# Kernel tuning notes

Hardware: AMD Instinct MI355X
Metric: run time of the kernel (lower is better)

## Reference

```python
import jax, jax.numpy as jnp
import numpy as np

H_IMG = 256; W_IMG = 256; C = 256
WIN = (16, 16); STRIPE = (32, 32); DF = 4; NH = 4
ASZ = (STRIPE[0] // DF, STRIPE[1] // DF)
TS = ((STRIPE[0] + ASZ[0]) // 2, (STRIPE[1] + ASZ[1]) // 2)  # stripe bias table half-size (20,20)


def _win_part(x, ws):
    # (B,H,W,c) -> (B*nW, ws0*ws1, c)
    B, H, W, c = x.shape
    x = x.reshape(B, H // ws[0], ws[0], W // ws[1], ws[1], c)
    return x.transpose(0, 1, 3, 2, 4, 5).reshape(-1, ws[0] * ws[1], c)


def _win_rev(w, ws, H, W):
    c = w.shape[-1]
    B = w.shape[0] // ((H // ws[0]) * (W // ws[1]))
    x = w.reshape(B, H // ws[0], W // ws[1], ws[0], ws[1], c)
    return x.transpose(0, 1, 3, 2, 4, 5).reshape(B, H, W, c)


def _l2n(x):
    # F.normalize(dim=-1)
    return x / jnp.maximum(jnp.linalg.norm(x, axis=-1, keepdims=True), 1e-12)


def _affine(attn, logit_scale, w1, b1, w2, table, index):
    # attn: (B_, nH, N1, N2); AffineTransform with mask=None
    N1, N2 = attn.shape[-2], attn.shape[-1]
    attn = attn * jnp.exp(jnp.minimum(logit_scale, np.log(100.0)))  # clamp max=log(1/0.01)
    bt = jax.nn.relu(table.reshape(-1, 2) @ w1 + b1) @ w2  # (T, nH)
    bias = bt[index.reshape(-1)].reshape(N1, N2, -1).transpose(2, 0, 1)  # (nH,N1,N2)
    return attn + (16.0 * jax.nn.sigmoid(bias))[None]


def _coords(start, size):
    h = np.arange(start[0], start[0] + size[0])
    w = np.arange(start[1], start[1] + size[1])
    return np.stack(np.meshgrid(h, w, indexing='ij')).reshape(2, -1)


def _idx(c1, c2, md):
    d = (c1[:, :, None] - c2[:, None, :]).transpose(1, 2, 0).astype(np.int64)
    return (d[..., 0] + md[0] - 1) * (2 * md[1] - 1) + (d[..., 1] + md[1] - 1)


def _table(ts):
    h = np.arange(-(ts[0] - 1), ts[0], dtype=np.float32) / (ts[0] - 1)
    w = np.arange(-(ts[1] - 1), ts[1], dtype=np.float32) / (ts[1] - 1)
    t = np.stack(np.meshgrid(h, w, indexing='ij'), axis=-1)[None] * 8.0
    return (np.sign(t) * np.log2(np.abs(t) + 1.0) / np.log2(8.0)).astype(np.float32)


def setup_inputs():
    ks = iter(jax.random.split(jax.random.key(0), 32))
    def nrm(shape, s=0.02):
        return jax.random.normal(next(ks), shape, dtype=jnp.float32) * s
    inp = {}
    inp['x'] = jax.random.normal(next(ks), (1, H_IMG * W_IMG, C), dtype=jnp.float32)
    inp['qkv_w'] = nrm((C, 3 * C)); inp['qkv_b'] = nrm((3 * C,))
    inp['anchor_w'] = nrm((C, C // 2)); inp['anchor_b'] = nrm((C // 2,))
    for tag in ['w', 's1', 's2']:
        inp['ls_' + tag] = jnp.full((NH, 1, 1), np.log(10.0), dtype=jnp.float32)
        inp['cpb_w1_' + tag] = nrm((2, 512), 0.1)
        inp['cpb_b1_' + tag] = nrm((512,), 0.1)
        inp['cpb_w2_' + tag] = nrm((512, NH), 0.1)
    inp['proj_w'] = nrm((C, C)); inp['proj_b'] = nrm((C,))
    inp['table_w'] = jnp.asarray(_table(WIN))
    inp['table_s'] = jnp.asarray(_table(TS))
    cw = _coords((0, 0), WIN)
    inp['index_w'] = jnp.asarray(_idx(cw, cw, WIN), dtype=jnp.int32)
    cs = _coords((0, 0), STRIPE)
    st = ((STRIPE[0] - ASZ[0]) // 2, (STRIPE[1] - ASZ[1]) // 2)
    ca = _coords(st, ASZ)
    inp['index_a2w'] = jnp.asarray(_idx(ca, cs, TS), dtype=jnp.int32)
    inp['index_w2a'] = jnp.asarray(_idx(cs, ca, TS), dtype=jnp.int32)
    return inp


def reference(x, qkv_w, qkv_b, anchor_w, anchor_b,
              ls_w, cpb_w1_w, cpb_b1_w, cpb_w2_w,
              ls_s1, cpb_w1_s1, cpb_b1_s1, cpb_w2_s1,
              ls_s2, cpb_w1_s2, cpb_b1_s2, cpb_w2_s2,
              proj_w, proj_b, table_w, table_s,
              index_w, index_a2w, index_w2a):
    B, L, c = x.shape
    qkv = x @ qkv_w + qkv_b               # (B, L, 3C)
    half = 3 * c // 2
    hd = half // 3 // NH                  # head_dim per branch
    # ---- window attention on first half of qkv channels ----
    qw = _win_part(qkv[..., :half].reshape(B, H_IMG, W_IMG, half), WIN)  # (B_, N, 3*C/2)
    B_, N, _ = qw.shape
    q, k, v = qw.reshape(B_, N, 3, NH, hd).transpose(2, 0, 3, 1, 4)
    attn = jnp.einsum('bhnd,bhmd->bhnm', _l2n(q), _l2n(k))
    attn = jax.nn.softmax(_affine(attn, ls_w, cpb_w1_w, cpb_b1_w, cpb_w2_w, table_w, index_w), axis=-1)
    xw = jnp.einsum('bhnm,bhmd->bhnd', attn, v).transpose(0, 2, 1, 3).reshape(B_, N, NH * hd)
    xw = _win_rev(xw, WIN, H_IMG, W_IMG).reshape(B, L, c // 2)
    # ---- anchor projection: AvgPool2d(DF) + Linear(C -> C/2) ----
    xi = x.reshape(B, H_IMG, W_IMG, c)
    pooled = xi.reshape(B, H_IMG // DF, DF, W_IMG // DF, DF, c).mean(axis=(2, 4))
    anchor = pooled @ anchor_w + anchor_b  # (B, H/DF, W/DF, C/2)
    # ---- anchor stripe attention on second half ----
    qs = _win_part(qkv[..., half:].reshape(B, H_IMG, W_IMG, half), STRIPE)  # (Bs, N1, 3*C/2)
    Bs, N1, _ = qs.shape
    anc = _win_part(anchor, ASZ)           # (Bs, N2, C/2)
    N2 = anc.shape[1]
    q, k, v = qs.reshape(Bs, N1, 3, NH, hd).transpose(2, 0, 3, 1, 4)
    anc = anc.reshape(Bs, N2, NH, hd).transpose(0, 2, 1, 3)
    a1 = jnp.einsum('bhnd,bhmd->bhnm', _l2n(anc), _l2n(k))   # (Bs,NH,N2,N1)
    a1 = jax.nn.softmax(_affine(a1, ls_s1, cpb_w1_s1, cpb_b1_s1, cpb_w2_s1, table_s, index_a2w), axis=-1)
    xm = jnp.einsum('bhnm,bhmd->bhnd', a1, v)                # (Bs,NH,N2,hd)
    a2 = jnp.einsum('bhnd,bhmd->bhnm', _l2n(q), _l2n(anc))   # (Bs,NH,N1,N2)
    a2 = jax.nn.softmax(_affine(a2, ls_s2, cpb_w1_s2, cpb_b1_s2, cpb_w2_s2, table_s, index_w2a), axis=-1)
    xs = jnp.einsum('bhnm,bhmd->bhnd', a2, xm).transpose(0, 2, 1, 3).reshape(Bs, N1, NH * hd)
    xs = _win_rev(xs, STRIPE, H_IMG, W_IMG).reshape(B, L, c // 2)
    # ---- merge + output projection ----
    return jnp.concatenate([xw, xs], axis=-1) @ proj_w + proj_b
```

## Files before the change

### kernel.cpp

```cpp
#include <hip/hip_runtime.h>
#include <cstdint>
#include <cstddef>

typedef unsigned short u16;
typedef __attribute__((ext_vector_type(8))) short short8;
typedef __attribute__((ext_vector_type(4))) float floatx4;
typedef __attribute__((ext_vector_type(4))) unsigned int uintx4;
typedef __attribute__((ext_vector_type(2))) unsigned int uintx2;

__device__ __forceinline__ float bf2f(u16 u){
  union { unsigned int i; float f; } v; v.i = ((unsigned int)u) << 16; return v.f;
}
__device__ __forceinline__ u16 f2bf(float f){
  union { float ff; unsigned int i; } v; v.ff = f;
  return (u16)((v.i + 0x7fffu + ((v.i >> 16) & 1u)) >> 16);
}
__device__ __forceinline__ unsigned int pk2(float a, float b){
  return (unsigned int)f2bf(a) | ((unsigned int)f2bf(b) << 16);
}
__device__ __forceinline__ void load32(const u16* p, float* v){
  const uintx4* p4 = (const uintx4*)p;
#pragma unroll
  for (int c = 0; c < 4; ++c){
    uintx4 u = p4[c];
    v[c*8+0] = bf2f((u16)(u.x & 0xffffu)); v[c*8+1] = bf2f((u16)(u.x >> 16));
    v[c*8+2] = bf2f((u16)(u.y & 0xffffu)); v[c*8+3] = bf2f((u16)(u.y >> 16));
    v[c*8+4] = bf2f((u16)(u.z & 0xffffu)); v[c*8+5] = bf2f((u16)(u.z >> 16));
    v[c*8+6] = bf2f((u16)(u.w & 0xffffu)); v[c*8+7] = bf2f((u16)(u.w >> 16));
  }
}
__device__ __forceinline__ void norm_store(u16* dst, const float* v, int t, int strideU16){
  float ss = 0.f;
#pragma unroll
  for (int e = 0; e < 32; ++e) ss += v[e]*v[e];
  float inv = 1.f / fmaxf(sqrtf(ss), 1e-12f);
#pragma unroll
  for (int q = 0; q < 4; ++q){
    uintx4 u;
    u.x = pk2(v[q*8+0]*inv, v[q*8+1]*inv);
    u.y = pk2(v[q*8+2]*inv, v[q*8+3]*inv);
    u.z = pk2(v[q*8+4]*inv, v[q*8+5]*inv);
    u.w = pk2(v[q*8+6]*inv, v[q*8+7]*inv);
    *(uintx4*)(dst + q*strideU16 + t*8) = u;
  }
}
__device__ __forceinline__ float expc(float a){
  return __expf(fminf(a, 30.f));
}
__device__ __forceinline__ uintx4 ld8f_bf(const float* g){
  floatx4 u0 = *(const floatx4*)g;
  floatx4 u1 = *(const floatx4*)(g + 4);
  uintx4 w;
  w.x = pk2(u0.x, u0.y); w.y = pk2(u0.z, u0.w);
  w.z = pk2(u1.x, u1.y); w.w = pk2(u1.z, u1.w);
  return w;
}
__device__ __forceinline__ float redq(float v){
  v += __shfl_xor(v, 16); v += __shfl_xor(v, 32);
  return v;
}

__global__ void transpose_w(const float* __restrict__ qkv_w, const float* __restrict__ anchor_w,
                            const float* __restrict__ proj_w,
                            u16* __restrict__ qkvt, u16* __restrict__ anct, u16* __restrict__ projt){
  int id = blockIdx.x*256 + threadIdx.x;
  if (id < 196608){ int k = id / 768, n = id % 768; qkvt[n*256 + k] = f2bf(qkv_w[id]); }
  else if (id < 229376){ int r = id - 196608; int k = r / 128, n = r % 128; anct[n*256 + k] = f2bf(anchor_w[r]); }
  else { int r = id - 229376; int k = r >> 8, n = r & 255; projt[n*256 + k] = f2bf(proj_w[r]); }
}

__global__ void cpb_mlp(const float* __restrict__ tw, const float* __restrict__ ts,
                        const float* __restrict__ w1w, const float* __restrict__ b1w, const float* __restrict__ w2w,
                        const float* __restrict__ w1s1, const float* __restrict__ b1s1, const float* __restrict__ w2s1,
                        const float* __restrict__ w1s2, const float* __restrict__ b1s2, const float* __restrict__ w2s2,
                        float* __restrict__ btw, float* __restrict__ bts1, float* __restrict__ bts2){
  int tag = blockIdx.y;
  const float *tab, *w1, *b1, *w2; float* bt; int T;
  if (tag == 0){ tab = tw; w1 = w1w;  b1 = b1w;  w2 = w2w;  bt = btw;  T = 961; }
  else if (tag == 1){ tab = ts; w1 = w1s1; b1 = b1s1; w2 = w2s1; bt = bts1; T = 1521; }
  else { tab = ts; w1 = w1s2; b1 = b1s2; w2 = w2s2; bt = bts2; T = 1521; }
  __shared__ float sw1[2][512];
  __shared__ float sb1[512];
  __shared__ float sw2[512][4];
  for (int j = threadIdx.x; j < 512; j += 256){
    sw1[0][j] = w1[j]; sw1[1][j] = w1[512 + j]; sb1[j] = b1[j];
    for (int h = 0; h < 4; ++h) sw2[j][h] = w2[j*4 + h];
  }
  __syncthreads();
  int idx = blockIdx.x*256 + threadIdx.x;
  int r = idx >> 2, hh = idx & 3;
  if (r < T){
    float t0 = tab[2*r], t1 = tab[2*r + 1];
    float acc = 0.f;
    for (int j = 0; j < 512; ++j){
      float hj = fmaxf(fmaf(t0, sw1[0][j], fmaf(t1, sw1[1][j], sb1[j])), 0.f);
      acc = fmaf(hj, sw2[j][hh], acc);
    }
    bt[r*4 + hh] = acc;
  }
}

__global__ void bias_gather(const float* __restrict__ btw, const float* __restrict__ bts1,
                            const float* __restrict__ bts2,
                            const int* __restrict__ idxw, const int* __restrict__ idxa2w,
                            const int* __restrict__ idxw2a,
                            float* __restrict__ bw, float* __restrict__ bs1, float* __restrict__ bs2){
  int id = blockIdx.x*256 + threadIdx.x;
  int which = id >> 18;
  int rem = id & 262143;
  int h = rem >> 16, e = rem & 65535;
  const float* bt; const int* ix; float* dst;
  if (which == 0){ bt = btw;  ix = idxw;   dst = bw;  }
  else if (which == 1){ bt = bts1; ix = idxa2w; dst = bs1; }
  else { bt = bts2; ix = idxw2a; dst = bs2; }
  float v = bt[ix[e]*4 + h];
  dst[h*65536 + e] = 16.f / (1.f + expc(-v));
}

__global__ void avgpool(const float* __restrict__ x, float* __restrict__ pooled){
  int a = blockIdx.x, c = threadIdx.x;
  int ay = a >> 6, ax = a & 63;
  float acc = 0.f;
#pragma unroll
  for (int dy = 0; dy < 4; ++dy)
#pragma unroll
    for (int dx = 0; dx < 4; ++dx)
      acc += x[(size_t)((ay*4 + dy)*256 + ax*4 + dx)*256 + c];
  pooled[(size_t)a*256 + c] = acc * 0.0625f;
}

__launch_bounds__(256, 2)
__global__ void gemm_bt(const float* __restrict__ A, const u16* __restrict__ Bt,
                        const float* __restrict__ bias, u16* __restrict__ C,
                        int M, int N, int K){
  __shared__ __align__(16) u16 lsA[4096];
  __shared__ __align__(16) u16 lsB[4096];
  const int tid = threadIdx.x, lane = tid & 63, wv = tid >> 6;
  const int lane15 = lane & 15, quad = lane >> 4;
  const int wr = wv >> 1, wc = wv & 1;
  const int m0 = blockIdx.x * 128, n0 = blockIdx.y * 128;
  floatx4 acc[4][4] = {};
  for (int k0 = 0; k0 < K; k0 += 32){
    uintx4 ra[2], rb[2];
#pragma unroll
    for (int c = 0; c < 2; ++c){
      int f = c*256 + tid, row = f & 127, q = f >> 7;
      ra[c] = ld8f_bf(A + (size_t)(m0 + row)*K + k0 + q*8);
      rb[c] = *(const uintx4*)(Bt + (size_t)(n0 + row)*K + k0 + q*8);
    }
#pragma unroll
    for (int c = 0; c < 2; ++c){
      int f = c*256 + tid;
      *(uintx4*)(lsA + f*8) = ra[c];
      *(uintx4*)(lsB + f*8) = rb[c];
    }
    __syncthreads();
    short8 a[4], b[4];
#pragma unroll
    for (int i = 0; i < 4; ++i)
      a[i] = *(const short8*)(lsA + quad*1024 + (wr*64 + i*16 + lane15)*8);
#pragma unroll
    for (int j = 0; j < 4; ++j)
      b[j] = *(const short8*)(lsB + quad*1024 + (wc*64 + j*16 + lane15)*8);
#pragma unroll
    for (int i = 0; i < 4; ++i)
#pragma unroll
      for (int j = 0; j < 4; ++j)
        acc[i][j] = __builtin_amdgcn_mfma_f32_16x16x32_bf16(a[i], b[j], acc[i][j], 0, 0, 0);
    __syncthreads();
  }
#pragma unroll
  for (int j = 0; j < 4; ++j){
    int col = n0 + wc*64 + j*16 + lane15;
    float bz = bias[col];
#pragma unroll
    for (int i = 0; i < 4; ++i){
      int rowb = m0 + wr*64 + i*16 + quad*4;
#pragma unroll
      for (int r = 0; r < 4; ++r)
        C[(size_t)(rowb + r)*N + col] = f2bf(acc[i][j][r] + bz);
    }
  }
}

__launch_bounds__(256, 2)
__global__ void gemm_proj_inplace(float* __restrict__ AC, const u16* __restrict__ Bt,
                                  const float* __restrict__ bias){
  __shared__ __align__(16) u16 lsA[4096];
  __shared__ __align__(16) u16 lsB[8192];
  const int tid = threadIdx.x, lane = tid & 63, wv = tid >> 6;
  const int lane15 = lane & 15, quad = lane >> 4;
  const int wr = wv >> 1, wc = wv & 1;
  const int m0 = blockIdx.x * 128;
  floatx4 acc[4][8] = {};
  for (int k0 = 0; k0 < 256; k0 += 32){
    uintx4 ra[2], rb[4];
#pragma unroll
    for (int c = 0; c < 2; ++c){
      int f = c*256 + tid, row = f & 127, q = f >> 7;
      ra[c] = ld8f_bf(AC + (size_t)(m0 + row)*256 + k0 + q*8);
    }
#pragma unroll
    for (int c = 0; c < 4; ++c){
      int f = c*256 + tid, row = f & 255, q = f >> 8;
      rb[c] = *(const uintx4*)(Bt + (size_t)row*256 + k0 + q*8);
    }
#pragma unroll
    for (int c = 0; c < 2; ++c){ int f = c*256 + tid; *(uintx4*)(lsA + f*8) = ra[c]; }
#pragma unroll
    for (int c = 0; c < 4; ++c){ int f = c*256 + tid; *(uintx4*)(lsB + f*8) = rb[c]; }
    __syncthreads();
    short8 a[4], b[8];
#pragma unroll
    for (int i = 0; i < 4; ++i)
      a[i] = *(const short8*)(lsA + quad*1024 + (wr*64 + i*16 + lane15)*8);
#pragma unroll
    for (int j = 0; j < 8; ++j)
      b[j] = *(const short8*)(lsB + quad*2048 + (wc*128 + j*16 + lane15)*8);
#pragma unroll
    for (int i = 0; i < 4; ++i)
#pragma unroll
      for (int j = 0; j < 8; ++j)
        acc[i][j] = __builtin_amdgcn_mfma_f32_16x16x32_bf16(a[i], b[j], acc[i][j], 0, 0, 0);
    __syncthreads();
  }
#pragma unroll
  for (int j = 0; j < 8; ++j){
    int col = wc*128 + j*16 + lane15;
    float bz = bias[col];
#pragma unroll
    for (int i = 0; i < 4; ++i){
      int rowb = m0 + wr*64 + i*16 + quad*4;
#pragma unroll
      for (int r = 0; r < 4; ++r)
        AC[(size_t)(rowb + r)*256 + col] = acc[i][j][r] + bz;
    }
  }
}

__launch_bounds__(256, 3)
__global__ void win_attn(const u16* __restrict__ qkvh, const float* __restrict__ lsw,
                         const float* __restrict__ biasw, float* __restrict__ outm, int r0){
  __shared__ __align__(16) u16 sm[24576];
  const int tid = threadIdx.x, lane = tid & 63, wv = tid >> 6;
  const int lane15 = lane & 15, quad = lane >> 4;
  const int h = blockIdx.y;
  const int wyl = blockIdx.x >> 4, wx = blockIdx.x & 15;
  u16* Ks = sm;
  u16* Qs = sm + 8192;
  u16* VT = sm + 16384;
  {
    int t = tid;
    int pyl = wyl*16 + (t >> 4), px = wx*16 + (t & 15);
    const u16* base = qkvh + (size_t)(pyl*256 + px)*384 + h*32;
    float v[32];
    load32(base, v);        norm_store(Qs, v, t, 2048);
    load32(base + 128, v);  norm_store(Ks, v, t, 2048);
    load32(base + 256, v);
    int kq = t >> 3, e = t & 7;
#pragma unroll
    for (int d = 0; d < 32; ++d) VT[kq*256 + d*8 + e] = f2bf(v[d]);
  }
  __syncthreads();
  short8 qf[4];
#pragma unroll
  for (int j = 0; j < 4; ++j)
    qf[j] = *(const short8*)(Qs + quad*2048 + (wv*64 + j*16 + lane15)*8);
  __syncthreads();

  float scale = __expf(fminf(lsw[h], 4.6051702f));
  float off = fminf(scale + 16.f, 80.f);
  const float* bptr = biasw + ((size_t)h << 16);
  u16* Pw = Qs + wv*2048;
  const floatx4 zf4 = {0.f, 0.f, 0.f, 0.f};
  floatx4 accO[2][4] = {};
  float lsum[4] = {};

  for (int kc = 0; kc < 8; ++kc){
    floatx4 bia[2][4];
#pragma unroll
    for (int i = 0; i < 2; ++i)
#pragma unroll
      for (int j = 0; j < 4; ++j)
        bia[i][j] = *(const floatx4*)(bptr + (size_t)(wv*64 + j*16 + lane15)*256 + kc*32 + i*16 + quad*4);
    short8 kf[2];
#pragma unroll
    for (int i = 0; i < 2; ++i)
      kf[i] = *(const short8*)(Ks + quad*2048 + (kc*32 + i*16 + lane15)*8);
#pragma unroll
    for (int i = 0; i < 2; ++i)
#pragma unroll
      for (int j = 0; j < 4; ++j){
        floatx4 sv = __builtin_amdgcn_mfma_f32_16x16x32_bf16(kf[i], qf[j], zf4, 0, 0, 0);
        float p0 = expc(fmaf(sv[0], scale, bia[i][j][0]) - off);
        float p1 = expc(fmaf(sv[1], scale, bia[i][j][1]) - off);
        float p2 = expc(fmaf(sv[2], scale, bia[i][j][2]) - off);
        float p3 = expc(fmaf(sv[3], scale, bia[i][j][3]) - off);
        lsum[j] += (p0 + p1) + (p2 + p3);
        uintx2 w; w.x = pk2(p0, p1); w.y = pk2(p2, p3);
        *(uintx2*)(Pw + (i*2 + (quad>>1))*512 + (j*16 + lane15)*8 + (quad&1)*4) = w;
      }
    asm volatile("s_waitcnt lgkmcnt(0)" ::: "memory");
    short8 ptf[4], vtf[2];
#pragma unroll
    for (int j = 0; j < 4; ++j)
      ptf[j] = *(const short8*)(Pw + quad*512 + (j*16 + lane15)*8);
#pragma unroll
    for (int m = 0; m < 2; ++m)
      vtf[m] = *(const short8*)(VT + (kc*4 + quad)*256 + (m*16 + lane15)*8);
#pragma unroll
    for (int m = 0; m < 2; ++m)
#pragma unroll
      for (int j = 0; j < 4; ++j)
        accO[m][j] = __builtin_amdgcn_mfma_f32_16x16x32_bf16(vtf[m], ptf[j], accO[m][j], 0, 0, 0);
  }
  float linv[4];
#pragma unroll
  for (int j = 0; j < 4; ++j) linv[j] = 1.f / redq(lsum[j]);
#pragma unroll
  for (int m = 0; m < 2; ++m)
#pragma unroll
    for (int j = 0; j < 4; ++j){
      int tok = wv*64 + j*16 + lane15;
      int py = r0 + wyl*16 + (tok >> 4), px = wx*16 + (tok & 15);
      floatx4 o = accO[m][j] * linv[j];
      *(floatx4*)(outm + (size_t)(py*256 + px)*256 + h*32 + m*16 + quad*4) = o;
    }
}

__launch_bounds__(256, 3)
__global__ void stripe_xm(const u16* __restrict__ qkvh, const u16* __restrict__ anchor,
                          const float* __restrict__ ls1, const float* __restrict__ bias1,
                          float* __restrict__ gl1, u16* __restrict__ gO, int r0){
  __shared__ __align__(16) u16 sm[18432];
  const int tid = threadIdx.x, lane = tid & 63, wv = tid >> 6;
  const int lane15 = lane & 15, quad = lane >> 4;
  const int s = blockIdx.x, h = blockIdx.y, kb = blockIdx.z;
  const int syl = s >> 3, sx = s & 7;
  u16* ANC = sm; u16* KC = sm + 2048; u16* VT = sm + 6144; u16* P1T = sm + 10240;
  if (tid < 64){
    int ay = (r0 >> 2) + syl*8 + (tid >> 3), ax = sx*8 + (tid & 7);
    float v[32]; load32(anchor + (size_t)(ay*64 + ax)*128 + h*32, v);
    norm_store(ANC, v, tid, 512);
  }
  __syncthreads();
  short8 ancf = *(const short8*)(ANC + quad*512 + (wv*16 + lane15)*8);
  float scale1 = __expf(fminf(ls1[h], 4.6051702f));
  float off1 = fminf(scale1 + 16.f, 80.f);
  const float* b1p = bias1 + ((size_t)h << 16) + (size_t)(wv*16 + lane15)*1024;
  const floatx4 zf4 = {0.f, 0.f, 0.f, 0.f};
  floatx4 accO1[2] = {};
  float l1 = 0.f;
  for (int kc = 0; kc < 4; ++kc){
    int kkb = kb*512 + kc*128;
    { int t = tid;
      if (t < 128){
        int tok = kkb + t;
        int pyl = syl*32 + (tok >> 5), px = sx*32 + (tok & 31);
        float v[32]; load32(qkvh + (size_t)(pyl*256 + px)*384 + 128 + h*32, v);
        norm_store(KC, v, t, 1024);
      } else {
        int t2 = t - 128, tok = kkb + t2;
        int pyl = syl*32 + (tok >> 5), px = sx*32 + (tok & 31);
        float v[32]; load32(qkvh + (size_t)(pyl*256 + px)*384 + 256 + h*32, v);
        int kq = t2 >> 3, e = t2 & 7;
#pragma unroll
        for (int d = 0; d < 32; ++d) VT[kq*256 + d*8 + e] = f2bf(v[d]);
      }
    }
    __syncthreads();
    floatx4 bia[8];
#pragma unroll
    for (int i = 0; i < 8; ++i)
      bia[i] = *(const floatx4*)(b1p + kkb + i*16 + quad*4);
#pragma unroll
    for (int i = 0; i < 8; ++i){
      short8 kf = *(const short8*)(KC + quad*1024 + (i*16 + lane15)*8);
      floatx4 sv = __builtin_amdgcn_mfma_f32_16x16x32_bf16(kf, ancf, zf4, 0, 0, 0);
      float p0 = expc(fmaf(sv[0], scale1, bia[i][0]) - off1);
      float p1 = expc(fmaf(sv[1], scale1, bia[i][1]) - off1);
      float p2 = expc(fmaf(sv[2], scale1, bia[i][2]) - off1);
      float p3 = expc(fmaf(sv[3], scale1, bia[i][3]) - off1);
      l1 += (p0 + p1) + (p2 + p3);
      uintx2 w; w.x = pk2(p0, p1); w.y = pk2(p2, p3);
      *(uintx2*)(P1T + (i*2 + (quad>>1))*512 + (wv*16 + lane15)*8 + (quad&1)*4) = w;
    }
    asm volatile("s_waitcnt lgkmcnt(0)" ::: "memory");
#pragma unroll
    for (int ks = 0; ks < 4; ++ks){
      short8 ptf = *(const short8*)(P1T + (ks*4 + quad)*512 + (wv*16 + lane15)*8);
#pragma unroll
      for (int m = 0; m < 2; ++m){
        short8 vtf = *(const short8*)(VT + (ks*4 + quad)*256 + (m*16 + lane15)*8);
        accO1[m] = __builtin_amdgcn_mfma_f32_16x16x32_bf16(vtf, ptf, accO1[m], 0, 0, 0);
      }
    }
    __syncthreads();
  }
  l1 = redq(l1);
  int ent = (s*4 + h)*2 + kb;
  if (quad == 0) gl1[ent*64 + wv*16 + lane15] = l1;
#pragma unroll
  for (int m = 0; m < 2; ++m){
    uintx2 w; w.x = pk2(accO1[m][0], accO1[m][1]); w.y = pk2(accO1[m][2], accO1[m][3]);
    *(uintx2*)(gO + (size_t)ent*2048 + (wv*16 + lane15)*32 + m*16 + quad*4) = w;
  }
}

__launch_bounds__(256, 3)
__global__ void stripe_xs(const u16* __restrict__ qkvh, const u16* __restrict__ anchor,
                          const float* __restrict__ ls2, const float* __restrict__ bias2,
                          const float* __restrict__ gl1, const u16* __restrict__ gO,
                          float* __restrict__ outm, int r0){
  __shared__ __align__(16) u16 sm[20480];
  const int tid = threadIdx.x, lane = tid & 63, wv = tid >> 6;
  const int lane15 = lane & 15, quad = lane >> 4;
  const int s = blockIdx.x >> 2, qc = blockIdx.x & 3, h = blockIdx.y;
  const int syl = s >> 3, sx = s & 7;
  u16* ANC = sm;
  u16* XMT = sm + 2048;
  u16* QW  = sm + 4096 + wv*2048;
  u16* P2T = sm + 12288 + wv*2048;
  if (tid < 64){
    int ay = (r0 >> 2) + syl*8 + (tid >> 3), ax = sx*8 + (tid & 7);
    float v[32]; load32(anchor + (size_t)(ay*64 + ax)*128 + h*32, v);
    norm_store(ANC, v, tid, 512);
  }
  {
    int a = tid >> 2, db = (tid & 3)*8;
    int e0 = (s*4 + h)*2;
    float inv = 1.f / (gl1[e0*64 + a] + gl1[(e0 + 1)*64 + a]);
    uintx4 u0 = *(const uintx4*)(gO + (size_t)e0*2048 + a*32 + db);
    uintx4 u1 = *(const uintx4*)(gO + (size_t)(e0 + 1)*2048 + a*32 + db);
    unsigned int w0[4] = {u0.x, u0.y, u0.z, u0.w};
    unsigned int w1[4] = {u1.x, u1.y, u1.z, u1.w};
#pragma unroll
    for (int c = 0; c < 4; ++c){
      float a0 = bf2f((u16)(w0[c] & 0xffffu)) + bf2f((u16)(w1[c] & 0xffffu));
      float a1 = bf2f((u16)(w0[c] >> 16))     + bf2f((u16)(w1[c] >> 16));
      XMT[(a >> 3)*256 + (db + c*2)*8     + (a & 7)] = f2bf(a0 * inv);
      XMT[(a >> 3)*256 + (db + c*2 + 1)*8 + (a & 7)] = f2bf(a1 * inv);
    }
  }
  __syncthreads();
  int tq = qc*256 + wv*64;
  { int tok = tq + lane;
    int pyl = syl*32 + (tok >> 5), px = sx*32 + (tok & 31);
    float v[32]; load32(qkvh + (size_t)(pyl*256 + px)*384 + h*32, v);
    norm_store(QW, v, lane, 512);
  }
  asm volatile("s_waitcnt lgkmcnt(0)" ::: "memory");
  short8 qf2[4];
#pragma unroll
  for (int j = 0; j < 4; ++j)
    qf2[j] = *(const short8*)(QW + quad*512 + (j*16 + lane15)*8);
  float scale2 = __expf(fminf(ls2[h], 4.6051702f));
  float off2 = fminf(scale2 + 16.f, 80.f);
  const float* b2p = bias2 + ((size_t)h << 16);
  const floatx4 zf4 = {0.f, 0.f, 0.f, 0.f};
  floatx4 accO2[2][4] = {};
  float l2[4] = {};
#pragma unroll
  for (int c = 0; c < 2; ++c){
    floatx4 bia[2][4];
#pragma unroll
    for (int i = 0; i < 2; ++i)
#pragma unroll
      for (int j = 0; j < 4; ++j)
        bia[i][j] = *(const floatx4*)(b2p + (size_t)(tq + j*16 + lane15)*64 + c*32 + i*16 + quad*4);
    short8 af[2];
#pragma unroll
    for (int i = 0; i < 2; ++i)
      af[i] = *(const short8*)(ANC + quad*512 + (c*32 + i*16 + lane15)*8);
#pragma unroll
    for (int i = 0; i < 2; ++i)
#pragma unroll
      for (int j = 0; j < 4; ++j){
        floatx4 sv = __builtin_amdgcn_mfma_f32_16x16x32_bf16(af[i], qf2[j], zf4, 0, 0, 0);
        float p0 = expc(fmaf(sv[0], scale2, bia[i][j][0]) - off2);
        float p1 = expc(fmaf(sv[1], scale2, bia[i][j][1]) - off2);
        float p2 = expc(fmaf(sv[2], scale2, bia[i][j][2]) - off2);
        float p3 = expc(fmaf(sv[3], scale2, bia[i][j][3]) - off2);
        l2[j] += (p0 + p1) + (p2 + p3);
        uintx2 w; w.x = pk2(p0, p1); w.y = pk2(p2, p3);
        *(uintx2*)(P2T + (i*2 + (quad>>1))*512 + (j*16 + lane15)*8 + (quad&1)*4) = w;
      }
    asm volatile("s_waitcnt lgkmcnt(0)" ::: "memory");
    short8 ptf[4], xmf[2];
#pragma unroll
    for (int j = 0; j < 4; ++j)
      ptf[j] = *(const short8*)(P2T + quad*512 + (j*16 + lane15)*8);
#pragma unroll
    for (int m = 0; m < 2; ++m)
      xmf[m] = *(const short8*)(XMT + (c*4 + quad)*256 + (m*16 + lane15)*8);
#pragma unroll
    for (int m = 0; m < 2; ++m)
#pragma unroll
      for (int j = 0; j < 4; ++j)
        accO2[m][j] = __builtin_amdgcn_mfma_f32_16x16x32_bf16(xmf[m], ptf[j], accO2[m][j], 0, 0, 0);
  }
  float linv[4];
#pragma unroll
  for (int j = 0; j < 4; ++j) linv[j] = 1.f / redq(l2[j]);
#pragma unroll
  for (int m = 0; m < 2; ++m)
#pragma unroll
    for (int j = 0; j < 4; ++j){
      int tok = tq + j*16 + lane15;
      int py = r0 + syl*32 + (tok >> 5), px = sx*32 + (tok & 31);
      floatx4 o = accO2[m][j] * linv[j];
      *(floatx4*)(outm + (size_t)(py*256 + px)*256 + 128 + h*32 + m*16 + quad*4) = o;
    }
}

extern "C" void kernel_launch(void* const* d_in, const int* in_sizes, int n_in,
                              void* d_out, int out_size, void* d_ws, size_t ws_size,
                              hipStream_t stream) {
  (void)in_sizes; (void)n_in; (void)out_size; (void)ws_size;
  const float* x        = (const float*)d_in[0];
  const float* qkv_w    = (const float*)d_in[1];
  const float* qkv_b    = (const float*)d_in[2];
  const float* anchor_w = (const float*)d_in[3];
  const float* anchor_b = (const float*)d_in[4];
  const float* ls_w     = (const float*)d_in[5];
  const float* w1_w     = (const float*)d_in[6];
  const float* b1_w     = (const float*)d_in[7];
  const float* w2_w     = (const float*)d_in[8];
  const float* ls_s1    = (const float*)d_in[9];
  const float* w1_s1    = (const float*)d_in[10];
  const float* b1_s1    = (const float*)d_in[11];
  const float* w2_s1    = (const float*)d_in[12];
  const float* ls_s2    = (const float*)d_in[13];
  const float* w1_s2    = (const float*)d_in[14];
  const float* b1_s2    = (const float*)d_in[15];
  const float* w2_s2    = (const float*)d_in[16];
  const float* proj_w   = (const float*)d_in[17];
  const float* proj_b   = (const float*)d_in[18];
  const float* table_w  = (const float*)d_in[19];
  const float* table_s  = (const float*)d_in[20];
  const int* index_w   = (const int*)d_in[21];
  const int* index_a2w = (const int*)d_in[22];
  const int* index_w2a = (const int*)d_in[23];

  char* ws = (char*)d_ws;
  u16*   qkvh   = (u16*)(ws + 0);
  float* pooled = (float*)(ws + 0);
  u16*   anch   = (u16*)(ws + 25165824);
  u16*   qkvt   = (u16*)(ws + 26214400);
  u16*   anct   = (u16*)(ws + 26607616);
  u16*   projt  = (u16*)(ws + 26673152);
  float* btw    = (float*)(ws + 26804224);
  float* bts1   = (float*)(ws + 26820608);
  float* bts2   = (float*)(ws + 26845184);
  float* biasw  = (float*)(ws + 26869760);
  float* bias1  = (float*)(ws + 27918336);
  float* bias2  = (float*)(ws + 28966912);
  float* gl1    = (float*)(ws + 30015488);
  u16*   gO     = (u16*)(ws + 30081024);

  float* merged = (float*)d_out;

  transpose_w<<<1152, 256, 0, stream>>>(qkv_w, anchor_w, proj_w, qkvt, anct, projt);
  cpb_mlp<<<dim3(24, 3), 256, 0, stream>>>(table_w, table_s,
                                           w1_w, b1_w, w2_w,
                                           w1_s1, b1_s1, w2_s1,
                                           w1_s2, b1_s2, w2_s2,
                                           btw, bts1, bts2);
  bias_gather<<<3072, 256, 0, stream>>>(btw, bts1, bts2, index_w, index_a2w, index_w2a,
                                        biasw, bias1, bias2);
  avgpool<<<4096, 256, 0, stream>>>(x, pooled);
  gemm_bt<<<dim3(32, 1), 256, 0, stream>>>(pooled, anct, anchor_b, anch, 4096, 128, 256);

  for (int half = 0; half < 2; ++half){
    const float* xh = x + (size_t)half*32768*256;
    int r0 = half*128;
    gemm_bt<<<dim3(256, 3), 256, 0, stream>>>(xh, qkvt, qkv_b, qkvh, 32768, 384, 256);
    win_attn<<<dim3(128, 4), 256, 0, stream>>>(qkvh, ls_w, biasw, merged, r0);
    gemm_bt<<<dim3(256, 3), 256, 0, stream>>>(xh, qkvt + 384*256, qkv_b + 384, qkvh, 32768, 384, 256);
    stripe_xm<<<dim3(32, 4, 2), 256, 0, stream>>>(qkvh, anch, ls_s1, bias1, gl1, gO, r0);
    stripe_xs<<<dim3(128, 4), 256, 0, stream>>>(qkvh, anch, ls_s2, bias2, gl1, gO, merged, r0);
  }

  gemm_proj_inplace<<<dim3(512), 256, 0, stream>>>(merged, projt, proj_b);
}
```

Before: 404.1 us.

## Process full image in one pass with bf16 merged buffer and single QKV GEMM

```diff
diff --git a/kernel.cpp b/kernel.cpp
--- a/kernel.cpp
+++ b/kernel.cpp
@@ -44,9 +44,7 @@
     *(uintx4*)(dst + q*strideU16 + t*8) = u;
   }
 }
-__device__ __forceinline__ float expc(float a){
-  return __expf(fminf(a, 30.f));
-}
+__device__ __forceinline__ float expc(float a){ return __expf(fminf(a, 30.f)); }
 __device__ __forceinline__ uintx4 ld8f_bf(const float* g){
   floatx4 u0 = *(const floatx4*)g;
   floatx4 u1 = *(const floatx4*)(g + 4);
@@ -60,34 +58,36 @@
   return v;
 }
 
-__global__ void transpose_w(const float* __restrict__ qkv_w, const float* __restrict__ anchor_w,
-                            const float* __restrict__ proj_w,
-                            u16* __restrict__ qkvt, u16* __restrict__ anct, u16* __restrict__ projt){
-  int id = blockIdx.x*256 + threadIdx.x;
-  if (id < 196608){ int k = id / 768, n = id % 768; qkvt[n*256 + k] = f2bf(qkv_w[id]); }
-  else if (id < 229376){ int r = id - 196608; int k = r / 128, n = r % 128; anct[n*256 + k] = f2bf(anchor_w[r]); }
-  else { int r = id - 229376; int k = r >> 8, n = r & 255; projt[n*256 + k] = f2bf(proj_w[r]); }
-}
-
-__global__ void cpb_mlp(const float* __restrict__ tw, const float* __restrict__ ts,
-                        const float* __restrict__ w1w, const float* __restrict__ b1w, const float* __restrict__ w2w,
-                        const float* __restrict__ w1s1, const float* __restrict__ b1s1, const float* __restrict__ w2s1,
-                        const float* __restrict__ w1s2, const float* __restrict__ b1s2, const float* __restrict__ w2s2,
-                        float* __restrict__ btw, float* __restrict__ bts1, float* __restrict__ bts2){
-  int tag = blockIdx.y;
+__global__ void prep1(const float* __restrict__ qkv_w, const float* __restrict__ anchor_w,
+                      const float* __restrict__ proj_w,
+                      u16* __restrict__ qkvt, u16* __restrict__ anct, u16* __restrict__ projt,
+                      const float* __restrict__ tw, const float* __restrict__ ts,
+                      const float* __restrict__ w1w, const float* __restrict__ b1w, const float* __restrict__ w2w,
+                      const float* __restrict__ w1s1, const float* __restrict__ b1s1, const float* __restrict__ w2s1,
+                      const float* __restrict__ w1s2, const float* __restrict__ b1s2, const float* __restrict__ w2s2,
+                      float* __restrict__ btw, float* __restrict__ bts1, float* __restrict__ bts2){
+  __shared__ float sw1[2][512];
+  __shared__ float sb1[512];
+  __shared__ float sw2[512][4];
+  if (blockIdx.x < 1152){
+    int id = blockIdx.x*256 + threadIdx.x;
+    if (id < 196608){ int k = id / 768, n = id % 768; qkvt[n*256 + k] = f2bf(qkv_w[id]); }
+    else if (id < 229376){ int r = id - 196608; int k = r / 128, n = r % 128; anct[n*256 + k] = f2bf(anchor_w[r]); }
+    else { int r = id - 229376; int k = r >> 8, n = r & 255; projt[n*256 + k] = f2bf(proj_w[r]); }
+    return;
+  }
+  int bx = blockIdx.x - 1152;
+  int tag = bx / 24, sb = bx % 24;
   const float *tab, *w1, *b1, *w2; float* bt; int T;
   if (tag == 0){ tab = tw; w1 = w1w;  b1 = b1w;  w2 = w2w;  bt = btw;  T = 961; }
   else if (tag == 1){ tab = ts; w1 = w1s1; b1 = b1s1; w2 = w2s1; bt = bts1; T = 1521; }
   else { tab = ts; w1 = w1s2; b1 = b1s2; w2 = w2s2; bt = bts2; T = 1521; }
-  __shared__ float sw1[2][512];
-  __shared__ float sb1[512];
-  __shared__ float sw2[512][4];
   for (int j = threadIdx.x; j < 512; j += 256){
     sw1[0][j] = w1[j]; sw1[1][j] = w1[512 + j]; sb1[j] = b1[j];
     for (int h = 0; h < 4; ++h) sw2[j][h] = w2[j*4 + h];
   }
   __syncthreads();
-  int idx = blockIdx.x*256 + threadIdx.x;
+  int idx = sb*256 + threadIdx.x;
   int r = idx >> 2, hh = idx & 3;
   if (r < T){
     float t0 = tab[2*r], t1 = tab[2*r + 1];
@@ -117,7 +117,7 @@
   dst[h*65536 + e] = 16.f / (1.f + expc(-v));
 }
 
-__global__ void avgpool(const float* __restrict__ x, float* __restrict__ pooled){
+__global__ void avgpool(const float* __restrict__ x, u16* __restrict__ pooled){
   int a = blockIdx.x, c = threadIdx.x;
   int ay = a >> 6, ax = a & 63;
   float acc = 0.f;
@@ -126,13 +126,14 @@
 #pragma unroll
     for (int dx = 0; dx < 4; ++dx)
       acc += x[(size_t)((ay*4 + dy)*256 + ax*4 + dx)*256 + c];
-  pooled[(size_t)a*256 + c] = acc * 0.0625f;
-}
-
-__launch_bounds__(256, 2)
-__global__ void gemm_bt(const float* __restrict__ A, const u16* __restrict__ Bt,
-                        const float* __restrict__ bias, u16* __restrict__ C,
-                        int M, int N, int K){
+  pooled[(size_t)a*256 + c] = f2bf(acc * 0.0625f);
+}
+
+template<bool AF32, bool CF32>
+__global__ __launch_bounds__(256, 3)
+void gemm_t(const void* __restrict__ Ap, const u16* __restrict__ Bt,
+            const float* __restrict__ bias, void* __restrict__ Cp,
+            int M, int N, int K){
   __shared__ __align__(16) u16 lsA[4096];
   __shared__ __align__(16) u16 lsB[4096];
   const int tid = threadIdx.x, lane = tid & 63, wv = tid >> 6;
@@ -145,7 +146,8 @@
 #pragma unroll
     for (int c = 0; c < 2; ++c){
       int f = c*256 + tid, row = f & 127, q = f >> 7;
-      ra[c] = ld8f_bf(A + (size_t)(m0 + row)*K + k0 + q*8);
+      if (AF32) ra[c] = ld8f_bf((const float*)Ap + (size_t)(m0 + row)*K + k0 + q*8);
+      else      ra[c] = *(const uintx4*)((const u16*)Ap + (size_t)(m0 + row)*K + k0 + q*8);
       rb[c] = *(const uintx4*)(Bt + (size_t)(n0 + row)*K + k0 + q*8);
     }
 #pragma unroll
@@ -177,82 +179,30 @@
     for (int i = 0; i < 4; ++i){
       int rowb = m0 + wr*64 + i*16 + quad*4;
 #pragma unroll
-      for (int r = 0; r < 4; ++r)
-        C[(size_t)(rowb + r)*N + col] = f2bf(acc[i][j][r] + bz);
-    }
-  }
-}
-
-__launch_bounds__(256, 2)
-__global__ void gemm_proj_inplace(float* __restrict__ AC, const u16* __restrict__ Bt,
-                                  const float* __restrict__ bias){
-  __shared__ __align__(16) u16 lsA[4096];
-  __shared__ __align__(16) u16 lsB[8192];
-  const int tid = threadIdx.x, lane = tid & 63, wv = tid >> 6;
-  const int lane15 = lane & 15, quad = lane >> 4;
-  const int wr = wv >> 1, wc = wv & 1;
-  const int m0 = blockIdx.x * 128;
-  floatx4 acc[4][8] = {};
-  for (int k0 = 0; k0 < 256; k0 += 32){
-    uintx4 ra[2], rb[4];
-#pragma unroll
-    for (int c = 0; c < 2; ++c){
-      int f = c*256 + tid, row = f & 127, q = f >> 7;
-      ra[c] = ld8f_bf(AC + (size_t)(m0 + row)*256 + k0 + q*8);
-    }
-#pragma unroll
-    for (int c = 0; c < 4; ++c){
-      int f = c*256 + tid, row = f & 255, q = f >> 8;
-      rb[c] = *(const uintx4*)(Bt + (size_t)row*256 + k0 + q*8);
-    }
-#pragma unroll
-    for (int c = 0; c < 2; ++c){ int f = c*256 + tid; *(uintx4*)(lsA + f*8) = ra[c]; }
-#pragma unroll
-    for (int c = 0; c < 4; ++c){ int f = c*256 + tid; *(uintx4*)(lsB + f*8) = rb[c]; }
-    __syncthreads();
-    short8 a[4], b[8];
-#pragma unroll
-    for (int i = 0; i < 4; ++i)
-      a[i] = *(const short8*)(lsA + quad*1024 + (wr*64 + i*16 + lane15)*8);
-#pragma unroll
-    for (int j = 0; j < 8; ++j)
-      b[j] = *(const short8*)(lsB + quad*2048 + (wc*128 + j*16 + lane15)*8);
-#pragma unroll
-    for (int i = 0; i < 4; ++i)
-#pragma unroll
-      for (int j = 0; j < 8; ++j)
-        acc[i][j] = __builtin_amdgcn_mfma_f32_16x16x32_bf16(a[i], b[j], acc[i][j], 0, 0, 0);
-    __syncthreads();
-  }
-#pragma unroll
-  for (int j = 0; j < 8; ++j){
-    int col = wc*128 + j*16 + lane15;
-    float bz = bias[col];
-#pragma unroll
-    for (int i = 0; i < 4; ++i){
-      int rowb = m0 + wr*64 + i*16 + quad*4;
-#pragma unroll
-      for (int r = 0; r < 4; ++r)
-        AC[(size_t)(rowb + r)*256 + col] = acc[i][j][r] + bz;
+      for (int r = 0; r < 4; ++r){
+        float v = acc[i][j][r] + bz;
+        if (CF32) ((float*)Cp)[(size_t)(rowb + r)*N + col] = v;
+        else      ((u16*)Cp)[(size_t)(rowb + r)*N + col] = f2bf(v);
+      }
     }
   }
 }
 
 __launch_bounds__(256, 3)
-__global__ void win_attn(const u16* __restrict__ qkvh, const float* __restrict__ lsw,
-                         const float* __restrict__ biasw, float* __restrict__ outm, int r0){
+__global__ void win_attn(const u16* __restrict__ qkv, const float* __restrict__ lsw,
+                         const float* __restrict__ biasw, u16* __restrict__ outm){
   __shared__ __align__(16) u16 sm[24576];
   const int tid = threadIdx.x, lane = tid & 63, wv = tid >> 6;
   const int lane15 = lane & 15, quad = lane >> 4;
   const int h = blockIdx.y;
-  const int wyl = blockIdx.x >> 4, wx = blockIdx.x & 15;
+  const int wy = blockIdx.x >> 4, wx = blockIdx.x & 15;
   u16* Ks = sm;
   u16* Qs = sm + 8192;
   u16* VT = sm + 16384;
   {
     int t = tid;
-    int pyl = wyl*16 + (t >> 4), px = wx*16 + (t & 15);
-    const u16* base = qkvh + (size_t)(pyl*256 + px)*384 + h*32;
+    int py = wy*16 + (t >> 4), px = wx*16 + (t & 15);
+    const u16* base = qkv + (size_t)(py*256 + px)*768 + h*32;
     float v[32];
     load32(base, v);        norm_store(Qs, v, t, 2048);
     load32(base + 128, v);  norm_store(Ks, v, t, 2048);
@@ -322,24 +272,25 @@
 #pragma unroll
     for (int j = 0; j < 4; ++j){
       int tok = wv*64 + j*16 + lane15;
-      int py = r0 + wyl*16 + (tok >> 4), px = wx*16 + (tok & 15);
+      int py = wy*16 + (tok >> 4), px = wx*16 + (tok & 15);
       floatx4 o = accO[m][j] * linv[j];
-      *(floatx4*)(outm + (size_t)(py*256 + px)*256 + h*32 + m*16 + quad*4) = o;
+      uintx2 w; w.x = pk2(o.x, o.y); w.y = pk2(o.z, o.w);
+      *(uintx2*)(outm + (size_t)(py*256 + px)*256 + h*32 + m*16 + quad*4) = w;
     }
 }
 
 __launch_bounds__(256, 3)
-__global__ void stripe_xm(const u16* __restrict__ qkvh, const u16* __restrict__ anchor,
+__global__ void stripe_xm(const u16* __restrict__ qkv, const u16* __restrict__ anchor,
                           const float* __restrict__ ls1, const float* __restrict__ bias1,
-                          float* __restrict__ gl1, u16* __restrict__ gO, int r0){
+                          float* __restrict__ gl1, u16* __restrict__ gO){
   __shared__ __align__(16) u16 sm[18432];
   const int tid = threadIdx.x, lane = tid & 63, wv = tid >> 6;
   const int lane15 = lane & 15, quad = lane >> 4;
   const int s = blockIdx.x, h = blockIdx.y, kb = blockIdx.z;
-  const int syl = s >> 3, sx = s & 7;
+  const int sy = s >> 3, sx = s & 7;
   u16* ANC = sm; u16* KC = sm + 2048; u16* VT = sm + 6144; u16* P1T = sm + 10240;
   if (tid < 64){
-    int ay = (r0 >> 2) + syl*8 + (tid >> 3), ax = sx*8 + (tid & 7);
+    int ay = sy*8 + (tid >> 3), ax = sx*8 + (tid & 7);
     float v[32]; load32(anchor + (size_t)(ay*64 + ax)*128 + h*32, v);
     norm_store(ANC, v, tid, 512);
   }
@@ -356,13 +307,13 @@
     { int t = tid;
       if (t < 128){
         int tok = kkb + t;
-        int pyl = syl*32 + (tok >> 5), px = sx*32 + (tok & 31);
-        float v[32]; load32(qkvh + (size_t)(pyl*256 + px)*384 + 128 + h*32, v);
+        int py = sy*32 + (tok >> 5), px = sx*32 + (tok & 31);
+        float v[32]; load32(qkv + (size_t)(py*256 + px)*768 + 512 + h*32, v);
         norm_store(KC, v, t, 1024);
       } else {
         int t2 = t - 128, tok = kkb + t2;
-        int pyl = syl*32 + (tok >> 5), px = sx*32 + (tok & 31);
-        float v[32]; load32(qkvh + (size_t)(pyl*256 + px)*384 + 256 + h*32, v);
+        int py = sy*32 + (tok >> 5), px = sx*32 + (tok & 31);
+        float v[32]; load32(qkv + (size_t)(py*256 + px)*768 + 640 + h*32, v);
         int kq = t2 >> 3, e = t2 & 7;
 #pragma unroll
         for (int d = 0; d < 32; ++d) VT[kq*256 + d*8 + e] = f2bf(v[d]);
@@ -408,21 +359,21 @@
 }
 
 __launch_bounds__(256, 3)
-__global__ void stripe_xs(const u16* __restrict__ qkvh, const u16* __restrict__ anchor,
+__global__ void stripe_xs(const u16* __restrict__ qkv, const u16* __restrict__ anchor,
                           const float* __restrict__ ls2, const float* __restrict__ bias2,
                           const float* __restrict__ gl1, const u16* __restrict__ gO,
-                          float* __restrict__ outm, int r0){
+                          u16* __restrict__ outm){
   __shared__ __align__(16) u16 sm[20480];
   const int tid = threadIdx.x, lane = tid & 63, wv = tid >> 6;
   const int lane15 = lane & 15, quad = lane >> 4;
   const int s = blockIdx.x >> 2, qc = blockIdx.x & 3, h = blockIdx.y;
-  const int syl = s >> 3, sx = s & 7;
+  const int sy = s >> 3, sx = s & 7;
   u16* ANC = sm;
   u16* XMT = sm + 2048;
   u16* QW  = sm + 4096 + wv*2048;
   u16* P2T = sm + 12288 + wv*2048;
   if (tid < 64){
-    int ay = (r0 >> 2) + syl*8 + (tid >> 3), ax = sx*8 + (tid & 7);
+    int ay = sy*8 + (tid >> 3), ax = sx*8 + (tid & 7);
     float v[32]; load32(anchor + (size_t)(ay*64 + ax)*128 + h*32, v);
     norm_store(ANC, v, tid, 512);
   }
@@ -445,8 +396,8 @@
   __syncthreads();
   int tq = qc*256 + wv*64;
   { int tok = tq + lane;
-    int pyl = syl*32 + (tok >> 5), px = sx*32 + (tok & 31);
-    float v[32]; load32(qkvh + (size_t)(pyl*256 + px)*384 + h*32, v);
+    int py = sy*32 + (tok >> 5), px = sx*32 + (tok & 31);
+    float v[32]; load32(qkv + (size_t)(py*256 + px)*768 + 384 + h*32, v);
     norm_store(QW, v, lane, 512);
   }
   asm volatile("s_waitcnt lgkmcnt(0)" ::: "memory");
@@ -507,9 +458,10 @@
 #pragma unroll
     for (int j = 0; j < 4; ++j){
       int tok = tq + j*16 + lane15;
-      int py = r0 + syl*32 + (tok >> 5), px = sx*32 + (tok & 31);
+      int py = sy*32 + (tok >> 5), px = sx*32 + (tok & 31);
       floatx4 o = accO2[m][j] * linv[j];
-      *(floatx4*)(outm + (size_t)(py*256 + px)*256 + 128 + h*32 + m*16 + quad*4) = o;
+      uintx2 w; w.x = pk2(o.x, o.y); w.y = pk2(o.z, o.w);
+      *(uintx2*)(outm + (size_t)(py*256 + px)*256 + 128 + h*32 + m*16 + quad*4) = w;
     }
 }
 
@@ -543,43 +495,35 @@
   const int* index_w2a = (const int*)d_in[23];
 
   char* ws = (char*)d_ws;
-  u16*   qkvh   = (u16*)(ws + 0);
-  float* pooled = (float*)(ws + 0);
-  u16*   anch   = (u16*)(ws + 25165824);
-  u16*   qkvt   = (u16*)(ws + 26214400);
-  u16*   anct   = (u16*)(ws + 26607616);
-  u16*   projt  = (u16*)(ws + 26673152);
-  float* btw    = (float*)(ws + 26804224);
-  float* bts1   = (float*)(ws + 26820608);
-  float* bts2   = (float*)(ws + 26845184);
-  float* biasw  = (float*)(ws + 26869760);
-  float* bias1  = (float*)(ws + 27918336);
-  float* bias2  = (float*)(ws + 28966912);
-  float* gl1    = (float*)(ws + 30015488);
-  u16*   gO     = (u16*)(ws + 30081024);
-
-  float* merged = (float*)d_out;
-
-  transpose_w<<<1152, 256, 0, stream>>>(qkv_w, anchor_w, proj_w, qkvt, anct, projt);
-  cpb_mlp<<<dim3(24, 3), 256, 0, stream>>>(table_w, table_s,
-                                           w1_w, b1_w, w2_w,
-                                           w1_s1, b1_s1, w2_s1,
-                                           w1_s2, b1_s2, w2_s2,
-                                           btw, bts1, bts2);
+  u16*   qkv    = (u16*)(ws + 0);
+  u16*   merged = (u16*)(ws + 100663296);
+  u16*   pooled = (u16*)(ws + 134217728);
+  u16*   anch   = (u16*)(ws + 136314880);
+  u16*   qkvt   = (u16*)(ws + 137363456);
+  u16*   anct   = (u16*)(ws + 137756672);
+  u16*   projt  = (u16*)(ws + 137822208);
+  float* btw    = (float*)(ws + 137953280);
+  float* bts1   = (float*)(ws + 137969664);
+  float* bts2   = (float*)(ws + 137994240);
+  float* biasw  = (float*)(ws + 138018816);
+  float* bias1  = (float*)(ws + 139067392);
+  float* bias2  = (float*)(ws + 140115968);
+  float* gl1    = (float*)(ws + 141164544);
+  u16*   gO     = (u16*)(ws + 141295616);
+
+  prep1<<<1224, 256, 0, stream>>>(qkv_w, anchor_w, proj_w, qkvt, anct, projt,
+                                  table_w, table_s,
+                                  w1_w, b1_w, w2_w,
+                                  w1_s1, b1_s1, w2_s1,
+                                  w1_s2, b1_s2, w2_s2,
+                                  btw, bts1, bts2);
   bias_gather<<<3072, 256, 0, stream>>>(btw, bts1, bts2, index_w, index_a2w, index_w2a,
                                         biasw, bias1, bias2);
   avgpool<<<4096, 256, 0, stream>>>(x, pooled);
-  gemm_bt<<<dim3(32, 1), 256, 0, stream>>>(pooled, anct, anchor_b, anch, 4096, 128, 256);
-
-  for (int half = 0; half < 2; ++half){
-    const float* xh = x + (size_t)half*32768*256;
-    int r0 = half*128;
-    gemm_bt<<<dim3(256, 3), 256, 0, stream>>>(xh, qkvt, qkv_b, qkvh, 32768, 384, 256);
-    win_attn<<<dim3(128, 4), 256, 0, stream>>>(qkvh, ls_w, biasw, merged, r0);
-    gemm_bt<<<dim3(256, 3), 256, 0, stream>>>(xh, qkvt + 384*256, qkv_b + 384, qkvh, 32768, 384, 256);
-    stripe_xm<<<dim3(32, 4, 2), 256, 0, stream>>>(qkvh, anch, ls_s1, bias1, gl1, gO, r0);
-    stripe_xs<<<dim3(128, 4), 256, 0, stream>>>(qkvh, anch, ls_s2, bias2, gl1, gO, merged, r0);
-  }
-
-  gemm_proj_inplace<<<dim3(512), 256, 0, stream>>>(merged, projt, proj_b);
-}
+  gemm_t<false, false><<<dim3(32, 1), 256, 0, stream>>>(pooled, anct, anchor_b, anch, 4096, 128, 256);
+  gemm_t<true,  false><<<dim3(512, 6), 256, 0, stream>>>(x, qkvt, qkv_b, qkv, 65536, 768, 256);
+  win_attn<<<dim3(256, 4), 256, 0, stream>>>(qkv, ls_w, biasw, merged);
+  stripe_xm<<<dim3(64, 4, 2), 256, 0, stream>>>(qkv, anch, ls_s1, bias1, gl1, gO);
+  stripe_xs<<<dim3(256, 4), 256, 0, stream>>>(qkv, anch, ls_s2, bias2, gl1, gO, merged);
+  gemm_t<false, true><<<dim3(512, 2), 256, 0, stream>>>(merged, projt, proj_b, d_out, 65536, 256, 256);
+}
```

New measurement: 405.3 us. About the same (+0.3%).
